# Performance work log

Measured on AMD Instinct MI355X. Metric: run time of the kernel, lower is better.

Reference implementation:

```python
import jax, jax.numpy as jnp
import numpy as np

HEADS = 4

def _topk_mask(attn, k):
    # exact replica of mask.scatter_(-1, topk_indices, 1.0): exactly k ones per row
    C = attn.shape[-1]
    _, idx = jax.lax.top_k(attn, k)                      # [b,h,C,k]
    return jax.nn.one_hot(idx, C, dtype=attn.dtype).sum(axis=-2) > 0  # [b,h,C,C] bool


def setup_inputs() -> dict:
    key = jax.random.key(0)
    ks = jax.random.split(key, 8)
    b, dim, h, w = 32, 128, 4096, 1
    s = 0.05
    return {
        "x": jax.random.normal(ks[0], (b, dim, h, w), jnp.float32),
        "qkv_w": jax.random.normal(ks[1], (3 * dim, dim), jnp.float32) * s,
        "qkv_b": jax.random.normal(ks[2], (3 * dim,), jnp.float32) * s,
        "dw_w": jax.random.normal(ks[3], (3 * dim, 1, 3, 3), jnp.float32) * s,
        "dw_b": jax.random.normal(ks[4], (3 * dim,), jnp.float32) * s,
        "proj_w": jax.random.normal(ks[5], (dim, dim), jnp.float32) * s,
        "proj_b": jax.random.normal(ks[6], (dim,), jnp.float32) * s,
        "temperature": jnp.ones((HEADS, 1, 1), jnp.float32),
        "attn_w": jnp.full((4,), 0.2, jnp.float32),  # attn1..attn4
    }


def reference(x, qkv_w, qkv_b, dw_w, dw_b, proj_w, proj_b, temperature, attn_w):
    b, c, h, w = x.shape
    # 1x1 conv qkv, then 3x3 depthwise conv (groups = 3*c)
    qkv = jnp.einsum('bchw,oc->bohw', x, qkv_w) + qkv_b[None, :, None, None]
    qkv = jax.lax.conv_general_dilated(
        qkv, dw_w, window_strides=(1, 1), padding=((1, 1), (1, 1)),
        dimension_numbers=('NCHW', 'OIHW', 'NCHW'), feature_group_count=3 * c
    ) + dw_b[None, :, None, None]
    q, k, v = jnp.split(qkv, 3, axis=1)
    heads = lambda t: t.reshape(b, HEADS, c // HEADS, h * w)  # b head c (hw)
    q, k, v = heads(q), heads(k), heads(v)
    # F.normalize(dim=-1), eps=1e-12
    q = q / jnp.maximum(jnp.linalg.norm(q, axis=-1, keepdims=True), 1e-12)
    k = k / jnp.maximum(jnp.linalg.norm(k, axis=-1, keepdims=True), 1e-12)
    C = c // HEADS
    attn = jnp.einsum('bhcn,bhdn->bhcd', q, k) * temperature[None]  # [b,head,C,C]
    top_ks = [C // 2, (2 * C) // 3, (3 * C) // 4, (4 * C) // 5]
    out = jnp.zeros_like(v)
    for i, kk in enumerate(top_ks):
        m = _topk_mask(attn, kk)
        a = jax.nn.softmax(jnp.where(m, attn, -jnp.inf), axis=-1)
        out = out + attn_w[i] * jnp.einsum('bhcd,bhdn->bhcn', a, v)
    out = out.reshape(b, c, h, w)
    out = jnp.einsum('bchw,oc->bohw', out, proj_w) + proj_b[None, :, None, None]
    return out
```

## Files before the change

### kernel.cpp

```cpp
#include <hip/hip_runtime.h>

#define B_ 32
#define CD 128
#define O3 384
#define N  4096
#define H_ 4
#define C_ 32

typedef __bf16 bf16x8 __attribute__((ext_vector_type(8)));
typedef float floatx4 __attribute__((ext_vector_type(4)));

#define MFMA16(a, b, c) __builtin_amdgcn_mfma_f32_16x16x32_bf16(a, b, c, 0, 0, 0)

__device__ __forceinline__ float b2f(unsigned int u) {
  return __builtin_bit_cast(float, u << 16);
}
__device__ __forceinline__ float b2fh(unsigned int u) {
  return __builtin_bit_cast(float, u & 0xffff0000u);
}
__device__ __forceinline__ unsigned short f2b(float f) {
  unsigned int bits = __builtin_bit_cast(unsigned int, f);
  unsigned int r = (bits + 0x7FFFu + ((bits >> 16) & 1u)) >> 16;
  return (unsigned short)r;
}

__global__ __launch_bounds__(256) void k0_xt(
    const float* __restrict__ x, unsigned short* __restrict__ xT,
    const float* __restrict__ qkv_w, const float* __restrict__ proj_w,
    const float* __restrict__ dw_w, const float* __restrict__ dw_b,
    unsigned short* __restrict__ qkv_wb, unsigned short* __restrict__ proj_wb,
    float4* __restrict__ dwq)
{
  __shared__ float xt[32 * 68];
  const int t = threadIdx.x;
  const int n0 = blockIdx.x * 64, c0 = blockIdx.y * 32, b = blockIdx.z;
  const float* xb = x + ((size_t)b * CD + c0) * N + n0;
#pragma unroll
  for (int i = 0; i < 2; i++) {
    int f = i * 256 + t;
    int c = f >> 4, n4 = (f & 15) * 4;
    float4 v = *(const float4*)(xb + (size_t)c * N + n4);
    *(float4*)&xt[c * 68 + n4] = v;
  }

  if (blockIdx.z == 0 && blockIdx.y < 2) {
    int wid = blockIdx.y * 64 + blockIdx.x;
    if (wid < 66) {
      int e = (wid * 256 + t) * 4;
      if (e < 49152) {
        float4 v = *(const float4*)(qkv_w + e);
        unsigned short tmp[4] = {f2b(v.x), f2b(v.y), f2b(v.z), f2b(v.w)};
        *(uint2*)(qkv_wb + e) = *(uint2*)tmp;
      } else if (e < 65536) {
        int off = e - 49152;
        float4 v = *(const float4*)(proj_w + off);
        unsigned short tmp[4] = {f2b(v.x), f2b(v.y), f2b(v.z), f2b(v.w)};
        *(uint2*)(proj_wb + off) = *(uint2*)tmp;
      } else {
        int o = (e - 65536) >> 2;
        if (o < 384)
          dwq[o] = make_float4(dw_w[o * 9 + 1], dw_w[o * 9 + 4],
                               dw_w[o * 9 + 7], dw_b[o]);
      }
    }
  }

  __syncthreads();
  int n = t >> 2, cb = (t & 3) * 8;
  unsigned short tmp[8];
#pragma unroll
  for (int j = 0; j < 8; j++) tmp[j] = f2b(xt[(cb + j) * 68 + n]);
  *(uint4*)(xT + ((size_t)b * N + n0 + n) * CD + c0 + cb) = *(uint4*)tmp;
}

__global__ __launch_bounds__(256, 4) void k1_qkv_dw(
    const unsigned short* __restrict__ xT, const unsigned short* __restrict__ qkv_wb,
    const float* __restrict__ qkv_b, const float4* __restrict__ dwq,
    unsigned short* __restrict__ qkvd, unsigned short* __restrict__ vT)
{
  __shared__ __align__(16) char smem[34816];
  unsigned short* Bs   = (unsigned short*)smem;
  unsigned short* pres = (unsigned short*)smem;

  const int t = threadIdx.x;
  const int otile = blockIdx.x, ytile = blockIdx.y, b = blockIdx.z;
  const int obase = otile * 128;
  const int ybase = ytile * 124;
  const int wv = t >> 6, l = t & 63, quad = l >> 4, lm = l & 15;
  const bool interior = (ytile >= 1 && ytile <= 32);

  const unsigned short* wbase =
      qkv_wb + (size_t)(obase + wv * 32 + lm) * CD + quad * 8;
  bf16x8 wa0[4], wa1[4];
#pragma unroll
  for (int ks = 0; ks < 4; ks++) {
    wa0[ks] = *(const bf16x8*)(wbase + ks * 32);
    wa1[ks] = *(const bf16x8*)(wbase + 16 * CD + ks * 32);
  }

  if (interior) {
#pragma unroll
    for (int i = 0; i < 8; i++) {
      int f = i * 256 + t;
      int row = f >> 4, c8 = (f & 15) * 8;
      *(uint4*)&Bs[row * 136 + c8] =
          *(const uint4*)(xT + ((size_t)b * N + ybase - 2 + row) * CD + c8);
    }
  } else {
#pragma unroll
    for (int i = 0; i < 8; i++) {
      int f = i * 256 + t;
      int row = f >> 4, c8 = (f & 15) * 8;
      int yg = ybase - 2 + row;
      uint4 v = make_uint4(0u, 0u, 0u, 0u);
      if (yg >= 0 && yg < N)
        v = *(const uint4*)(xT + ((size_t)b * N + yg) * CD + c8);
      *(uint4*)&Bs[row * 136 + c8] = v;
    }
  }
  __syncthreads();

  floatx4 acc[2][8];
#pragma unroll
  for (int mt = 0; mt < 2; mt++)
#pragma unroll
    for (int nt = 0; nt < 8; nt++) acc[mt][nt] = (floatx4){0.f, 0.f, 0.f, 0.f};

#pragma unroll
  for (int ks = 0; ks < 4; ks++) {
#pragma unroll
    for (int nt = 0; nt < 8; nt++) {
      bf16x8 bb = *(const bf16x8*)&Bs[(nt * 16 + lm) * 136 + ks * 32 + quad * 8];
      acc[0][nt] = MFMA16(wa0[ks], bb, acc[0][nt]);
      acc[1][nt] = MFMA16(wa1[ks], bb, acc[1][nt]);
    }
  }

  if (otile < 2) {
    __syncthreads();
    if (interior) {
#pragma unroll
      for (int mt = 0; mt < 2; mt++)
#pragma unroll
        for (int r = 0; r < 4; r++) {
          int o = wv * 32 + mt * 16 + quad * 4 + r;
          float bias = qkv_b[obase + o];
#pragma unroll
          for (int nt = 0; nt < 8; nt++) {
            int i = nt * 16 + lm;
            if (i >= 1) pres[o * 132 + (i - 1)] = f2b(acc[mt][nt][r] + bias);
          }
        }
    } else {
#pragma unroll
      for (int mt = 0; mt < 2; mt++)
#pragma unroll
        for (int r = 0; r < 4; r++) {
          int o = wv * 32 + mt * 16 + quad * 4 + r;
          float bias = qkv_b[obase + o];
#pragma unroll
          for (int nt = 0; nt < 8; nt++) {
            int i = nt * 16 + lm;
            if (i >= 1) {
              int yg = ybase - 2 + i;
              pres[o * 132 + (i - 1)] =
                  f2b((yg >= 0 && yg < N) ? (acc[mt][nt][r] + bias) : 0.f);
            }
          }
        }
    }
    __syncthreads();
    const int p = t & 63, og = t >> 6;
    const bool ok = (p < 62) && (ybase + 2 * p < N);
    const unsigned int* presu = (const unsigned int*)pres;
    for (int r2 = 0; r2 < 32; r2++) {
      int oo = __builtin_amdgcn_readfirstlane(obase + og * 32 + r2);
      float4 wq = dwq[oo];
      int o = oo - obase;
      unsigned int u0 = presu[o * 66 + p];
      unsigned int u1 = presu[o * 66 + p + 1];
      float v0 = b2f(u0), v1 = b2fh(u0), v2 = b2f(u1), v3 = b2fh(u1);
      float out0 = wq.x * v0 + wq.y * v1 + wq.z * v2 + wq.w;
      float out1 = wq.x * v1 + wq.y * v2 + wq.z * v3 + wq.w;
      unsigned int pk = (unsigned int)f2b(out0) |
                        ((unsigned int)f2b(out1) << 16);
      if (ok)
        *(unsigned int*)(qkvd + ((size_t)b * 256 + oo) * N + ybase + 2 * p) = pk;
    }
  } else {
    const int op = t & 63, quarter = t >> 6;
    const int o0 = 2 * op;
    const float4 wqa = dwq[256 + o0];
    const float4 wqb = dwq[256 + o0 + 1];
    __syncthreads();
    if (interior) {
#pragma unroll
      for (int mt = 0; mt < 2; mt++)
#pragma unroll
        for (int r = 0; r < 4; r++) {
          int o2 = wv * 32 + mt * 16 + quad * 4 + r;
          float bias = qkv_b[obase + o2];
#pragma unroll
          for (int nt = 0; nt < 8; nt++) {
            int i = nt * 16 + lm;
            pres[i * 132 + o2] = f2b(acc[mt][nt][r] + bias);
          }
        }
    } else {
#pragma unroll
      for (int mt = 0; mt < 2; mt++)
#pragma unroll
        for (int r = 0; r < 4; r++) {
          int o2 = wv * 32 + mt * 16 + quad * 4 + r;
          float bias = qkv_b[obase + o2];
#pragma unroll
          for (int nt = 0; nt < 8; nt++) {
            int i = nt * 16 + lm;
            int yg = ybase - 2 + i;
            pres[i * 132 + o2] =
                f2b((yg >= 0 && yg < N) ? (acc[mt][nt][r] + bias) : 0.f);
          }
        }
    }
    __syncthreads();
    const unsigned int* pu = (const unsigned int*)pres;
    int i0 = 2 + quarter * 31;
    unsigned int pm = pu[(i0 - 1) * 66 + op];
    unsigned int pc = pu[i0 * 66 + op];
    if (interior) {
      for (int i = i0; i < i0 + 31; i++) {
        unsigned int pp = pu[(i + 1) * 66 + op];
        int yo = ybase - 2 + i;
        float a0 = wqa.x * b2f(pm) + wqa.y * b2f(pc) + wqa.z * b2f(pp) + wqa.w;
        float a1 = wqb.x * b2fh(pm) + wqb.y * b2fh(pc) + wqb.z * b2fh(pp) + wqb.w;
        unsigned int pk = (unsigned int)f2b(a0) | ((unsigned int)f2b(a1) << 16);
        *(unsigned int*)(vT + ((size_t)b * N + yo) * CD + o0) = pk;
        pm = pc; pc = pp;
      }
    } else {
      for (int i = i0; i < i0 + 31; i++) {
        unsigned int pp = pu[(i + 1) * 66 + op];
        int yo = ybase - 2 + i;
        if (yo >= 0 && yo < N) {
          float a0 = wqa.x * b2f(pm) + wqa.y * b2f(pc) + wqa.z * b2f(pp) + wqa.w;
          float a1 = wqb.x * b2fh(pm) + wqb.y * b2fh(pc) + wqb.z * b2fh(pp) + wqb.w;
          unsigned int pk = (unsigned int)f2b(a0) | ((unsigned int)f2b(a1) << 16);
          *(unsigned int*)(vT + ((size_t)b * N + yo) * CD + o0) = pk;
        }
        pm = pc; pc = pp;
      }
    }
  }
}

__global__ __launch_bounds__(256, 4) void k3_gram(
    const unsigned short* __restrict__ qkvd, float* __restrict__ part)
{
  __shared__ float red[4 * 8 * 272];
  const int ns = blockIdx.x, h = blockIdx.y, b = blockIdx.z;
  const int t = threadIdx.x;
  const int wv = t >> 6, l = t & 63, quad = l >> 4, lm = l & 15;
  const unsigned short* qb = qkvd + ((size_t)b * 256 + h * C_) * N;
  const unsigned short* kb = qkvd + ((size_t)b * 256 + 128 + h * C_) * N;

  floatx4 acc[8];
#pragma unroll
  for (int i = 0; i < 8; i++) acc[i] = (floatx4){0.f, 0.f, 0.f, 0.f};

  const int nbase = ns * 512 + wv * 32 + quad * 8;
#pragma unroll
  for (int ch = 0; ch < 4; ch++) {
    int nc = nbase + ch * 128;
    bf16x8 a0 = *(const bf16x8*)(qb + (size_t)lm * N + nc);
    bf16x8 a1 = *(const bf16x8*)(qb + (size_t)(16 + lm) * N + nc);
    bf16x8 b0 = *(const bf16x8*)(kb + (size_t)lm * N + nc);
    bf16x8 b1 = *(const bf16x8*)(kb + (size_t)(16 + lm) * N + nc);
    acc[0] = MFMA16(a0, b0, acc[0]);
    acc[1] = MFMA16(a0, b1, acc[1]);
    acc[2] = MFMA16(a1, b0, acc[2]);
    acc[3] = MFMA16(a1, b1, acc[3]);
    acc[4] = MFMA16(a0, a0, acc[4]);
    acc[5] = MFMA16(a1, a1, acc[5]);
    acc[6] = MFMA16(b0, b0, acc[6]);
    acc[7] = MFMA16(b1, b1, acc[7]);
  }

#pragma unroll
  for (int tl = 0; tl < 8; tl++)
#pragma unroll
    for (int r = 0; r < 4; r++)
      red[wv * 2176 + tl * 272 + (quad * 4 + r) * 17 + lm] = acc[tl][r];
  __syncthreads();

  float* pb = part + ((size_t)(b * H_ + h) * 8 + ns) * 2048;
  for (int e = t; e < 2048; e += 256) {
    int tl = e >> 8, rc = e & 255, row = rc >> 4, col = rc & 15;
    int a = tl * 272 + row * 17 + col;
    float s = red[a] + red[2176 + a] + red[2 * 2176 + a] + red[3 * 2176 + a];
    if (tl < 4) {
      int mt = tl >> 1, nt = tl & 1;
      pb[(mt * 16 + row) * 32 + nt * 16 + col] = s;
    } else if (row == col) {
      if (tl < 6) pb[1024 + (tl - 4) * 16 + row] = s;
      else        pb[1056 + (tl - 6) * 16 + row] = s;
    }
  }
}

__global__ __launch_bounds__(256) void k45(
    const float* __restrict__ part, const unsigned short* __restrict__ proj_wb,
    const float* __restrict__ temperature, const float* __restrict__ attn_w,
    unsigned short* __restrict__ Mb)
{
  __shared__ float La[H_][C_][33];
  __shared__ float sq2[256];
  __shared__ float rn[256];
  __shared__ float exL[H_][C_][33];
  __shared__ unsigned char rkL[H_][C_][C_];
  __shared__ unsigned short AwtT[H_][C_][40];
  const int b = blockIdx.x, t = threadIdx.x;

  const float* pbb = part + (size_t)b * 65536;
  for (int e = t; e < 4 * 2048; e += 256) {
    int h = e >> 11, idx = e & 2047;
    if (idx < 1088) {
      const float* p = pbb + h * 16384 + idx;
      float s = 0.f;
#pragma unroll
      for (int j = 0; j < 8; j++) s += p[j * 2048];
      if (idx < 1024) La[h][idx >> 5][idx & 31] = s;
      else if (idx < 1056) sq2[h * 32 + (idx - 1024)] = s;
      else sq2[128 + h * 32 + (idx - 1056)] = s;
    }
  }
  __syncthreads();
  rn[t] = 1.f / fmaxf(sqrtf(sq2[t]), 1e-12f);
  __syncthreads();
  for (int e = t; e < 4096; e += 256) {
    int h = e >> 10, i = (e >> 5) & 31, j = e & 31;
    La[h][i][j] *= rn[h * 32 + i] * rn[128 + h * 32 + j] * temperature[h];
  }
  __syncthreads();

  if (t < 128) {
    int h = t >> 5, i = t & 31;
    float m = -1e30f;
    for (int j = 0; j < 32; j++) m = fmaxf(m, La[h][i][j]);
    float S0 = 0.f, S1 = 0.f, S2 = 0.f, S3 = 0.f;
    for (int j = 0; j < 32; j++) {
      float vj = La[h][i][j];
      int r = 0;
      for (int j2 = 0; j2 < 32; j2++) {
        float v2 = La[h][i][j2];
        r += (v2 > vj) || (v2 == vj && j2 < j);
      }
      float e = __expf(vj - m);
      exL[h][i][j] = e;
      rkL[h][i][j] = (unsigned char)r;
      if (r < 16) S0 += e;
      if (r < 21) S1 += e;
      if (r < 24) S2 += e;
      if (r < 25) S3 += e;
    }
    float w0 = attn_w[0] / S0, w1 = attn_w[1] / S1;
    float w2 = attn_w[2] / S2, w3 = attn_w[3] / S3;
    for (int j = 0; j < 32; j++) {
      int r = rkL[h][i][j];
      float cmb = (r < 16 ? w0 : 0.f) + (r < 21 ? w1 : 0.f) +
                  (r < 24 ? w2 : 0.f) + (r < 25 ? w3 : 0.f);
      AwtT[h][j][i] = f2b(exL[h][i][j] * cmb);
    }
  }
  __syncthreads();

  {
    const int wv = t >> 6, l = t & 63, quad = l >> 4, lm = l & 15;
    const int h = wv;
    bf16x8 bfr[2];
#pragma unroll
    for (int jt = 0; jt < 2; jt++)
      bfr[jt] = *(const bf16x8*)&AwtT[h][jt * 16 + lm][quad * 8];
#pragma unroll
    for (int mt = 0; mt < 8; mt++) {
      bf16x8 a = *(const bf16x8*)(proj_wb +
                    (size_t)(mt * 16 + lm) * CD + h * C_ + quad * 8);
#pragma unroll
      for (int jt = 0; jt < 2; jt++) {
        floatx4 acc = (floatx4){0.f, 0.f, 0.f, 0.f};
        acc = MFMA16(a, bfr[jt], acc);
#pragma unroll
        for (int r = 0; r < 4; r++) {
          int row = quad * 4 + r;
          Mb[(size_t)b * 16384 + (mt * 16 + row) * CD + h * C_ + jt * 16 + lm] =
              f2b(acc[r]);
        }
      }
    }
  }
}

__global__ __launch_bounds__(256, 4) void k6_out(
    const unsigned short* __restrict__ vT, const unsigned short* __restrict__ Mb,
    const float* __restrict__ proj_b, float* __restrict__ out)
{
  __shared__ unsigned short Bs[128 * 136];
  const int t = threadIdx.x;
  const int y0 = blockIdx.x * 128, b = blockIdx.y;
  const int wv = t >> 6, l = t & 63, quad = l >> 4, lm = l & 15;

#pragma unroll
  for (int i = 0; i < 8; i++) {
    int f = i * 256 + t;
    int row = f >> 4, c8 = (f & 15) * 8;
    *(uint4*)&Bs[row * 136 + c8] =
        *(const uint4*)(vT + ((size_t)b * N + y0 + row) * CD + c8);
  }
  __syncthreads();

  floatx4 acc[2][8];
#pragma unroll
  for (int mt = 0; mt < 2; mt++)
#pragma unroll
    for (int nt = 0; nt < 8; nt++) acc[mt][nt] = (floatx4){0.f, 0.f, 0.f, 0.f};

  const unsigned short* mbase =
      Mb + (size_t)b * 16384 + (size_t)(wv * 32 + lm) * CD + quad * 8;
#pragma unroll
  for (int ks = 0; ks < 4; ks++) {
    bf16x8 a0 = *(const bf16x8*)(mbase + ks * 32);
    bf16x8 a1 = *(const bf16x8*)(mbase + 16 * CD + ks * 32);
#pragma unroll
    for (int nt = 0; nt < 8; nt++) {
      bf16x8 bb = *(const bf16x8*)&Bs[(nt * 16 + lm) * 136 + ks * 32 + quad * 8];
      acc[0][nt] = MFMA16(a0, bb, acc[0][nt]);
      acc[1][nt] = MFMA16(a1, bb, acc[1][nt]);
    }
  }

#pragma unroll
  for (int mt = 0; mt < 2; mt++)
#pragma unroll
    for (int r = 0; r < 4; r++) {
      int o = wv * 32 + mt * 16 + quad * 4 + r;
      float pb = proj_b[o];
#pragma unroll
      for (int nt = 0; nt < 8; nt++) {
        int y = y0 + nt * 16 + lm;
        out[((size_t)b * CD + o) * N + y] = acc[mt][nt][r] + pb;
      }
    }
}

extern "C" void kernel_launch(void* const* d_in, const int* in_sizes, int n_in,
                              void* d_out, int out_size, void* d_ws, size_t ws_size,
                              hipStream_t stream)
{
  (void)in_sizes; (void)n_in; (void)out_size; (void)ws_size;
  const float* x           = (const float*)d_in[0];
  const float* qkv_w       = (const float*)d_in[1];
  const float* qkv_b       = (const float*)d_in[2];
  const float* dw_w        = (const float*)d_in[3];
  const float* dw_b        = (const float*)d_in[4];
  const float* proj_w      = (const float*)d_in[5];
  const float* proj_b      = (const float*)d_in[6];
  const float* temperature = (const float*)d_in[7];
  const float* attn_w      = (const float*)d_in[8];
  float* out = (float*)d_out;

  unsigned short* xT      = (unsigned short*)d_ws;
  unsigned short* qkv_wb  = xT + (size_t)16777216;
  unsigned short* proj_wb = qkv_wb + 49152;
  unsigned short* qkvd    = proj_wb + 16384;
  unsigned short* vT      = qkvd + (size_t)33554432;
  unsigned short* Mb      = vT + (size_t)16777216;
  float* part = (float*)xT;
  float4* dwq = (float4*)Mb;

  k0_xt    <<<dim3(64, 4, 32),  256, 0, stream>>>(x, xT, qkv_w, proj_w, dw_w,
                                                  dw_b, qkv_wb, proj_wb, dwq);
  k1_qkv_dw<<<dim3(3, 34, 32),  256, 0, stream>>>(xT, qkv_wb, qkv_b, dwq,
                                                  qkvd, vT);
  k3_gram  <<<dim3(8, H_, B_),  256, 0, stream>>>(qkvd, part);
  k45      <<<dim3(B_),         256, 0, stream>>>(part, proj_wb, temperature,
                                                  attn_w, Mb);
  k6_out   <<<dim3(32, B_),     256, 0, stream>>>(vT, Mb, proj_b, out);
}
```

Baseline: 251.4 us.

## Fuse Gram-matrix computation into QKV/depthwise kernel via atomics, drop qkvd round-trip

The q/k path of the QKV+depthwise kernel now computes 62-row tiles with all 256 q/k channels per block. It applies the depthwise conv in registers using lane shuffles, with the bias folded into a precomputed constant and edge corrections at the sequence ends. It then computes the per-head QK^T and squared-norm Gram partials with MFMA and atomically accumulates them into a small buffer zeroed in k0. This removes the separate k3_gram kernel, the 64MB bf16 qkvd write/read, and the 8-way partial reduction in k45. The costs are atomic contention, a lower occupancy bound, and nondeterministic float summation order.

```diff
diff --git a/kernel.cpp b/kernel.cpp
--- a/kernel.cpp
+++ b/kernel.cpp
@@ -28,8 +28,11 @@
     const float* __restrict__ x, unsigned short* __restrict__ xT,
     const float* __restrict__ qkv_w, const float* __restrict__ proj_w,
     const float* __restrict__ dw_w, const float* __restrict__ dw_b,
+    const float* __restrict__ qkv_b,
     unsigned short* __restrict__ qkv_wb, unsigned short* __restrict__ proj_wb,
-    float4* __restrict__ dwq)
+    float4* __restrict__ dwq, float4* __restrict__ dwq2,
+    float* __restrict__ c0a, float* __restrict__ c2a,
+    float* __restrict__ part2)
 {
   __shared__ float xt[32 * 68];
   const int t = threadIdx.x;
@@ -62,6 +65,18 @@
           dwq[o] = make_float4(dw_w[o * 9 + 1], dw_w[o * 9 + 4],
                                dw_w[o * 9 + 7], dw_b[o]);
       }
+    } else if (wid == 66) {
+      int o = t;
+      float w0 = dw_w[o * 9 + 1], w1 = dw_w[o * 9 + 4], w2 = dw_w[o * 9 + 7];
+      float qb = qkv_b[o];
+      dwq2[o] = make_float4(w0, w1, w2, qb * (w0 + w1 + w2) + dw_b[o]);
+      c0a[o] = qb * w0;
+      c2a[o] = qb * w2;
+    } else {
+      int idx = (wid - 67) * 256 + t;
+      uint4 z4 = make_uint4(0u, 0u, 0u, 0u);
+      for (int k2 = idx; k2 < 34816; k2 += 61 * 256)
+        ((uint4*)part2)[k2] = z4;
     }
   }
 
@@ -73,121 +88,212 @@
   *(uint4*)(xT + ((size_t)b * N + n0 + n) * CD + c0 + cb) = *(uint4*)tmp;
 }
 
-__global__ __launch_bounds__(256, 4) void k1_qkv_dw(
+__global__ __launch_bounds__(256, 3) void k1_qkv_dw(
     const unsigned short* __restrict__ xT, const unsigned short* __restrict__ qkv_wb,
     const float* __restrict__ qkv_b, const float4* __restrict__ dwq,
-    unsigned short* __restrict__ qkvd, unsigned short* __restrict__ vT)
+    const float4* __restrict__ dwq2, const float* __restrict__ c0a,
+    const float* __restrict__ c2a, unsigned short* __restrict__ vT,
+    float* part2)
 {
   __shared__ __align__(16) char smem[34816];
-  unsigned short* Bs   = (unsigned short*)smem;
-  unsigned short* pres = (unsigned short*)smem;
-
   const int t = threadIdx.x;
-  const int otile = blockIdx.x, ytile = blockIdx.y, b = blockIdx.z;
-  const int obase = otile * 128;
-  const int ybase = ytile * 124;
+  const int b = blockIdx.y;
   const int wv = t >> 6, l = t & 63, quad = l >> 4, lm = l & 15;
-  const bool interior = (ytile >= 1 && ytile <= 32);
-
-  const unsigned short* wbase =
-      qkv_wb + (size_t)(obase + wv * 32 + lm) * CD + quad * 8;
-  bf16x8 wa0[4], wa1[4];
-#pragma unroll
-  for (int ks = 0; ks < 4; ks++) {
-    wa0[ks] = *(const bf16x8*)(wbase + ks * 32);
-    wa1[ks] = *(const bf16x8*)(wbase + 16 * CD + ks * 32);
-  }
-
-  if (interior) {
-#pragma unroll
-    for (int i = 0; i < 8; i++) {
-      int f = i * 256 + t;
-      int row = f >> 4, c8 = (f & 15) * 8;
-      *(uint4*)&Bs[row * 136 + c8] =
-          *(const uint4*)(xT + ((size_t)b * N + ybase - 2 + row) * CD + c8);
+
+  if (blockIdx.x < 67) {
+    unsigned short* Bs    = (unsigned short*)smem;
+    unsigned short* pres2 = (unsigned short*)smem;
+    const int yw = blockIdx.x;
+    const int ybase = yw * 62;
+    const bool interior = (yw >= 1 && yw <= 65);
+
+    const unsigned short* wbase = qkv_wb + (size_t)(wv * 64 + lm) * CD + quad * 8;
+    bf16x8 wa[4][4];
+#pragma unroll
+    for (int mt = 0; mt < 4; mt++)
+#pragma unroll
+      for (int ks = 0; ks < 4; ks++)
+        wa[mt][ks] = *(const bf16x8*)(wbase + (size_t)mt * 16 * CD + ks * 32);
+
+    if (interior) {
+#pragma unroll
+      for (int i = 0; i < 4; i++) {
+        int f = i * 256 + t;
+        int row = f >> 4, c8 = (f & 15) * 8;
+        *(uint4*)&Bs[row * 136 + c8] =
+            *(const uint4*)(xT + ((size_t)b * N + ybase - 1 + row) * CD + c8);
+      }
+    } else {
+#pragma unroll
+      for (int i = 0; i < 4; i++) {
+        int f = i * 256 + t;
+        int row = f >> 4, c8 = (f & 15) * 8;
+        int yg = ybase - 1 + row;
+        uint4 v = make_uint4(0u, 0u, 0u, 0u);
+        if (yg >= 0 && yg < N)
+          v = *(const uint4*)(xT + ((size_t)b * N + yg) * CD + c8);
+        *(uint4*)&Bs[row * 136 + c8] = v;
+      }
+    }
+    __syncthreads();
+
+    floatx4 acc[4][4];
+#pragma unroll
+    for (int mt = 0; mt < 4; mt++)
+#pragma unroll
+      for (int nt = 0; nt < 4; nt++) acc[mt][nt] = (floatx4){0.f, 0.f, 0.f, 0.f};
+
+#pragma unroll
+    for (int ks = 0; ks < 4; ks++) {
+      bf16x8 bb[4];
+#pragma unroll
+      for (int nt = 0; nt < 4; nt++)
+        bb[nt] = *(const bf16x8*)&Bs[(nt * 16 + lm) * 136 + ks * 32 + quad * 8];
+#pragma unroll
+      for (int mt = 0; mt < 4; mt++)
+#pragma unroll
+        for (int nt = 0; nt < 4; nt++)
+          acc[mt][nt] = MFMA16(wa[mt][ks], bb[nt], acc[mt][nt]);
+    }
+    __syncthreads();
+
+    const int i1 = (l & 48) | ((lm + 1) & 15);
+    const int i2 = (l & 48) | ((lm + 2) & 15);
+#pragma unroll
+    for (int mt = 0; mt < 4; mt++) {
+#pragma unroll
+      for (int r = 0; r < 4; r++) {
+        int o = wv * 64 + mt * 16 + quad * 4 + r;
+        float4 wq = dwq2[o];
+        float cc0 = 0.f, cc2 = 0.f;
+        if (yw == 0)  cc0 = c0a[o];
+        if (yw == 66) cc2 = c2a[o];
+        float vv[5], r1[5], r2[5];
+#pragma unroll
+        for (int nt = 0; nt < 4; nt++) vv[nt] = acc[mt][nt][r];
+        vv[4] = 0.f;
+#pragma unroll
+        for (int nt = 0; nt < 4; nt++) {
+          r1[nt] = __shfl(vv[nt], i1);
+          r2[nt] = __shfl(vv[nt], i2);
+        }
+        r1[4] = 0.f; r2[4] = 0.f;
+#pragma unroll
+        for (int nt = 0; nt < 4; nt++) {
+          int p = nt * 16 + lm;
+          int y = ybase + p;
+          float g1 = (lm == 15) ? r1[nt + 1] : r1[nt];
+          float g2 = (lm >= 14) ? r2[nt + 1] : r2[nt];
+          float val = wq.x * vv[nt] + wq.y * g1 + wq.z * g2 + wq.w;
+          if (y == 0)     val -= cc0;
+          if (y == N - 1) val -= cc2;
+          bool ok = (p < 62) && (y < N);
+          pres2[o * 68 + p] = f2b(ok ? val : 0.f);
+        }
+      }
+    }
+    __syncthreads();
+
+    const int h = wv;
+    const unsigned short* pq = pres2 + (size_t)(h * 32) * 68;
+    const unsigned short* pk = pres2 + (size_t)(128 + h * 32) * 68;
+    floatx4 gqk[2][2], gqq[2], gkk[2];
+#pragma unroll
+    for (int a = 0; a < 2; a++) {
+      gqq[a] = (floatx4){0.f, 0.f, 0.f, 0.f};
+      gkk[a] = (floatx4){0.f, 0.f, 0.f, 0.f};
+#pragma unroll
+      for (int c = 0; c < 2; c++) gqk[a][c] = (floatx4){0.f, 0.f, 0.f, 0.f};
+    }
+#pragma unroll
+    for (int kc = 0; kc < 2; kc++) {
+      bf16x8 qf[2], kf[2];
+#pragma unroll
+      for (int tt = 0; tt < 2; tt++) {
+        qf[tt] = *(const bf16x8*)&pq[(tt * 16 + lm) * 68 + kc * 32 + quad * 8];
+        kf[tt] = *(const bf16x8*)&pk[(tt * 16 + lm) * 68 + kc * 32 + quad * 8];
+      }
+#pragma unroll
+      for (int tq = 0; tq < 2; tq++)
+#pragma unroll
+        for (int tk = 0; tk < 2; tk++)
+          gqk[tq][tk] = MFMA16(qf[tq], kf[tk], gqk[tq][tk]);
+      gqq[0] = MFMA16(qf[0], qf[0], gqq[0]);
+      gqq[1] = MFMA16(qf[1], qf[1], gqq[1]);
+      gkk[0] = MFMA16(kf[0], kf[0], gkk[0]);
+      gkk[1] = MFMA16(kf[1], kf[1], gkk[1]);
+    }
+    float* pp = part2 + ((size_t)b * H_ + h) * 1088;
+#pragma unroll
+    for (int tq = 0; tq < 2; tq++)
+#pragma unroll
+      for (int tk = 0; tk < 2; tk++)
+#pragma unroll
+        for (int r = 0; r < 4; r++)
+          atomicAdd(&pp[(tq * 16 + quad * 4 + r) * 32 + tk * 16 + lm],
+                    gqk[tq][tk][r]);
+    if (quad == (lm >> 2)) {
+      int r = lm & 3;
+      atomicAdd(&pp[1024 + lm],      gqq[0][r]);
+      atomicAdd(&pp[1024 + 16 + lm], gqq[1][r]);
+      atomicAdd(&pp[1056 + lm],      gkk[0][r]);
+      atomicAdd(&pp[1056 + 16 + lm], gkk[1][r]);
     }
   } else {
-#pragma unroll
-    for (int i = 0; i < 8; i++) {
-      int f = i * 256 + t;
-      int row = f >> 4, c8 = (f & 15) * 8;
-      int yg = ybase - 2 + row;
-      uint4 v = make_uint4(0u, 0u, 0u, 0u);
-      if (yg >= 0 && yg < N)
-        v = *(const uint4*)(xT + ((size_t)b * N + yg) * CD + c8);
-      *(uint4*)&Bs[row * 136 + c8] = v;
-    }
-  }
-  __syncthreads();
-
-  floatx4 acc[2][8];
-#pragma unroll
-  for (int mt = 0; mt < 2; mt++)
-#pragma unroll
-    for (int nt = 0; nt < 8; nt++) acc[mt][nt] = (floatx4){0.f, 0.f, 0.f, 0.f};
-
-#pragma unroll
-  for (int ks = 0; ks < 4; ks++) {
-#pragma unroll
-    for (int nt = 0; nt < 8; nt++) {
-      bf16x8 bb = *(const bf16x8*)&Bs[(nt * 16 + lm) * 136 + ks * 32 + quad * 8];
-      acc[0][nt] = MFMA16(wa0[ks], bb, acc[0][nt]);
-      acc[1][nt] = MFMA16(wa1[ks], bb, acc[1][nt]);
-    }
-  }
-
-  if (otile < 2) {
+    unsigned short* Bs   = (unsigned short*)smem;
+    unsigned short* pres = (unsigned short*)smem;
+    const int ytile = blockIdx.x - 67;
+    const int obase = 256;
+    const int ybase = ytile * 124;
+    const bool interior = (ytile >= 1 && ytile <= 32);
+
+    const unsigned short* wbase =
+        qkv_wb + (size_t)(obase + wv * 32 + lm) * CD + quad * 8;
+    bf16x8 wa0[4], wa1[4];
+#pragma unroll
+    for (int ks = 0; ks < 4; ks++) {
+      wa0[ks] = *(const bf16x8*)(wbase + ks * 32);
+      wa1[ks] = *(const bf16x8*)(wbase + 16 * CD + ks * 32);
+    }
+
+    if (interior) {
+#pragma unroll
+      for (int i = 0; i < 8; i++) {
+        int f = i * 256 + t;
+        int row = f >> 4, c8 = (f & 15) * 8;
+        *(uint4*)&Bs[row * 136 + c8] =
+            *(const uint4*)(xT + ((size_t)b * N + ybase - 2 + row) * CD + c8);
+      }
+    } else {
+#pragma unroll
+      for (int i = 0; i < 8; i++) {
+        int f = i * 256 + t;
+        int row = f >> 4, c8 = (f & 15) * 8;
+        int yg = ybase - 2 + row;
+        uint4 v = make_uint4(0u, 0u, 0u, 0u);
+        if (yg >= 0 && yg < N)
+          v = *(const uint4*)(xT + ((size_t)b * N + yg) * CD + c8);
+        *(uint4*)&Bs[row * 136 + c8] = v;
+      }
+    }
     __syncthreads();
-    if (interior) {
-#pragma unroll
-      for (int mt = 0; mt < 2; mt++)
-#pragma unroll
-        for (int r = 0; r < 4; r++) {
-          int o = wv * 32 + mt * 16 + quad * 4 + r;
-          float bias = qkv_b[obase + o];
-#pragma unroll
-          for (int nt = 0; nt < 8; nt++) {
-            int i = nt * 16 + lm;
-            if (i >= 1) pres[o * 132 + (i - 1)] = f2b(acc[mt][nt][r] + bias);
-          }
-        }
-    } else {
-#pragma unroll
-      for (int mt = 0; mt < 2; mt++)
-#pragma unroll
-        for (int r = 0; r < 4; r++) {
-          int o = wv * 32 + mt * 16 + quad * 4 + r;
-          float bias = qkv_b[obase + o];
-#pragma unroll
-          for (int nt = 0; nt < 8; nt++) {
-            int i = nt * 16 + lm;
-            if (i >= 1) {
-              int yg = ybase - 2 + i;
-              pres[o * 132 + (i - 1)] =
-                  f2b((yg >= 0 && yg < N) ? (acc[mt][nt][r] + bias) : 0.f);
-            }
-          }
-        }
-    }
-    __syncthreads();
-    const int p = t & 63, og = t >> 6;
-    const bool ok = (p < 62) && (ybase + 2 * p < N);
-    const unsigned int* presu = (const unsigned int*)pres;
-    for (int r2 = 0; r2 < 32; r2++) {
-      int oo = __builtin_amdgcn_readfirstlane(obase + og * 32 + r2);
-      float4 wq = dwq[oo];
-      int o = oo - obase;
-      unsigned int u0 = presu[o * 66 + p];
-      unsigned int u1 = presu[o * 66 + p + 1];
-      float v0 = b2f(u0), v1 = b2fh(u0), v2 = b2f(u1), v3 = b2fh(u1);
-      float out0 = wq.x * v0 + wq.y * v1 + wq.z * v2 + wq.w;
-      float out1 = wq.x * v1 + wq.y * v2 + wq.z * v3 + wq.w;
-      unsigned int pk = (unsigned int)f2b(out0) |
-                        ((unsigned int)f2b(out1) << 16);
-      if (ok)
-        *(unsigned int*)(qkvd + ((size_t)b * 256 + oo) * N + ybase + 2 * p) = pk;
-    }
-  } else {
+
+    floatx4 acc[2][8];
+#pragma unroll
+    for (int mt = 0; mt < 2; mt++)
+#pragma unroll
+      for (int nt = 0; nt < 8; nt++) acc[mt][nt] = (floatx4){0.f, 0.f, 0.f, 0.f};
+
+#pragma unroll
+    for (int ks = 0; ks < 4; ks++) {
+#pragma unroll
+      for (int nt = 0; nt < 8; nt++) {
+        bf16x8 bb = *(const bf16x8*)&Bs[(nt * 16 + lm) * 136 + ks * 32 + quad * 8];
+        acc[0][nt] = MFMA16(wa0[ks], bb, acc[0][nt]);
+        acc[1][nt] = MFMA16(wa1[ks], bb, acc[1][nt]);
+      }
+    }
+
     const int op = t & 63, quarter = t >> 6;
     const int o0 = 2 * op;
     const float4 wqa = dwq[256 + o0];
@@ -229,86 +335,32 @@
     unsigned int pc = pu[i0 * 66 + op];
     if (interior) {
       for (int i = i0; i < i0 + 31; i++) {
-        unsigned int pp = pu[(i + 1) * 66 + op];
+        unsigned int pp2 = pu[(i + 1) * 66 + op];
         int yo = ybase - 2 + i;
-        float a0 = wqa.x * b2f(pm) + wqa.y * b2f(pc) + wqa.z * b2f(pp) + wqa.w;
-        float a1 = wqb.x * b2fh(pm) + wqb.y * b2fh(pc) + wqb.z * b2fh(pp) + wqb.w;
-        unsigned int pk = (unsigned int)f2b(a0) | ((unsigned int)f2b(a1) << 16);
-        *(unsigned int*)(vT + ((size_t)b * N + yo) * CD + o0) = pk;
-        pm = pc; pc = pp;
+        float a0 = wqa.x * b2f(pm) + wqa.y * b2f(pc) + wqa.z * b2f(pp2) + wqa.w;
+        float a1 = wqb.x * b2fh(pm) + wqb.y * b2fh(pc) + wqb.z * b2fh(pp2) + wqb.w;
+        unsigned int pk2 = (unsigned int)f2b(a0) | ((unsigned int)f2b(a1) << 16);
+        *(unsigned int*)(vT + ((size_t)b * N + yo) * CD + o0) = pk2;
+        pm = pc; pc = pp2;
       }
     } else {
       for (int i = i0; i < i0 + 31; i++) {
-        unsigned int pp = pu[(i + 1) * 66 + op];
+        unsigned int pp2 = pu[(i + 1) * 66 + op];
         int yo = ybase - 2 + i;
         if (yo >= 0 && yo < N) {
-          float a0 = wqa.x * b2f(pm) + wqa.y * b2f(pc) + wqa.z * b2f(pp) + wqa.w;
-          float a1 = wqb.x * b2fh(pm) + wqb.y * b2fh(pc) + wqb.z * b2fh(pp) + wqb.w;
-          unsigned int pk = (unsigned int)f2b(a0) | ((unsigned int)f2b(a1) << 16);
-          *(unsigned int*)(vT + ((size_t)b * N + yo) * CD + o0) = pk;
+          float a0 = wqa.x * b2f(pm) + wqa.y * b2f(pc) + wqa.z * b2f(pp2) + wqa.w;
+          float a1 = wqb.x * b2fh(pm) + wqb.y * b2fh(pc) + wqb.z * b2fh(pp2) + wqb.w;
+          unsigned int pk2 = (unsigned int)f2b(a0) | ((unsigned int)f2b(a1) << 16);
+          *(unsigned int*)(vT + ((size_t)b * N + yo) * CD + o0) = pk2;
         }
-        pm = pc; pc = pp;
-      }
-    }
-  }
-}
-
-__global__ __launch_bounds__(256, 4) void k3_gram(
-    const unsigned short* __restrict__ qkvd, float* __restrict__ part)
-{
-  __shared__ float red[4 * 8 * 272];
-  const int ns = blockIdx.x, h = blockIdx.y, b = blockIdx.z;
-  const int t = threadIdx.x;
-  const int wv = t >> 6, l = t & 63, quad = l >> 4, lm = l & 15;
-  const unsigned short* qb = qkvd + ((size_t)b * 256 + h * C_) * N;
-  const unsigned short* kb = qkvd + ((size_t)b * 256 + 128 + h * C_) * N;
-
-  floatx4 acc[8];
-#pragma unroll
-  for (int i = 0; i < 8; i++) acc[i] = (floatx4){0.f, 0.f, 0.f, 0.f};
-
-  const int nbase = ns * 512 + wv * 32 + quad * 8;
-#pragma unroll
-  for (int ch = 0; ch < 4; ch++) {
-    int nc = nbase + ch * 128;
-    bf16x8 a0 = *(const bf16x8*)(qb + (size_t)lm * N + nc);
-    bf16x8 a1 = *(const bf16x8*)(qb + (size_t)(16 + lm) * N + nc);
-    bf16x8 b0 = *(const bf16x8*)(kb + (size_t)lm * N + nc);
-    bf16x8 b1 = *(const bf16x8*)(kb + (size_t)(16 + lm) * N + nc);
-    acc[0] = MFMA16(a0, b0, acc[0]);
-    acc[1] = MFMA16(a0, b1, acc[1]);
-    acc[2] = MFMA16(a1, b0, acc[2]);
-    acc[3] = MFMA16(a1, b1, acc[3]);
-    acc[4] = MFMA16(a0, a0, acc[4]);
-    acc[5] = MFMA16(a1, a1, acc[5]);
-    acc[6] = MFMA16(b0, b0, acc[6]);
-    acc[7] = MFMA16(b1, b1, acc[7]);
-  }
-
-#pragma unroll
-  for (int tl = 0; tl < 8; tl++)
-#pragma unroll
-    for (int r = 0; r < 4; r++)
-      red[wv * 2176 + tl * 272 + (quad * 4 + r) * 17 + lm] = acc[tl][r];
-  __syncthreads();
-
-  float* pb = part + ((size_t)(b * H_ + h) * 8 + ns) * 2048;
-  for (int e = t; e < 2048; e += 256) {
-    int tl = e >> 8, rc = e & 255, row = rc >> 4, col = rc & 15;
-    int a = tl * 272 + row * 17 + col;
-    float s = red[a] + red[2176 + a] + red[2 * 2176 + a] + red[3 * 2176 + a];
-    if (tl < 4) {
-      int mt = tl >> 1, nt = tl & 1;
-      pb[(mt * 16 + row) * 32 + nt * 16 + col] = s;
-    } else if (row == col) {
-      if (tl < 6) pb[1024 + (tl - 4) * 16 + row] = s;
-      else        pb[1056 + (tl - 6) * 16 + row] = s;
+        pm = pc; pc = pp2;
+      }
     }
   }
 }
 
 __global__ __launch_bounds__(256) void k45(
-    const float* __restrict__ part, const unsigned short* __restrict__ proj_wb,
+    const float* __restrict__ part2, const unsigned short* __restrict__ proj_wb,
     const float* __restrict__ temperature, const float* __restrict__ attn_w,
     unsigned short* __restrict__ Mb)
 {
@@ -320,19 +372,15 @@
   __shared__ unsigned short AwtT[H_][C_][40];
   const int b = blockIdx.x, t = threadIdx.x;
 
-  const float* pbb = part + (size_t)b * 65536;
-  for (int e = t; e < 4 * 2048; e += 256) {
-    int h = e >> 11, idx = e & 2047;
-    if (idx < 1088) {
-      const float* p = pbb + h * 16384 + idx;
-      float s = 0.f;
-#pragma unroll
-      for (int j = 0; j < 8; j++) s += p[j * 2048];
+  const float* pbb = part2 + (size_t)b * H_ * 1088;
+#pragma unroll
+  for (int h = 0; h < H_; h++)
+    for (int idx = t; idx < 1088; idx += 256) {
+      float s = pbb[h * 1088 + idx];
       if (idx < 1024) La[h][idx >> 5][idx & 31] = s;
       else if (idx < 1056) sq2[h * 32 + (idx - 1024)] = s;
       else sq2[128 + h * 32 + (idx - 1056)] = s;
     }
-  }
   __syncthreads();
   rn[t] = 1.f / fmaxf(sqrtf(sq2[t]), 1e-12f);
   __syncthreads();
@@ -470,18 +518,21 @@
   unsigned short* xT      = (unsigned short*)d_ws;
   unsigned short* qkv_wb  = xT + (size_t)16777216;
   unsigned short* proj_wb = qkv_wb + 49152;
-  unsigned short* qkvd    = proj_wb + 16384;
-  unsigned short* vT      = qkvd + (size_t)33554432;
+  unsigned short* hole    = proj_wb + 16384;
+  unsigned short* vT      = hole + (size_t)33554432;
   unsigned short* Mb      = vT + (size_t)16777216;
-  float* part = (float*)xT;
-  float4* dwq = (float4*)Mb;
-
-  k0_xt    <<<dim3(64, 4, 32),  256, 0, stream>>>(x, xT, qkv_w, proj_w, dw_w,
-                                                  dw_b, qkv_wb, proj_wb, dwq);
-  k1_qkv_dw<<<dim3(3, 34, 32),  256, 0, stream>>>(xT, qkv_wb, qkv_b, dwq,
-                                                  qkvd, vT);
-  k3_gram  <<<dim3(8, H_, B_),  256, 0, stream>>>(qkvd, part);
-  k45      <<<dim3(B_),         256, 0, stream>>>(part, proj_wb, temperature,
-                                                  attn_w, Mb);
-  k6_out   <<<dim3(32, B_),     256, 0, stream>>>(vT, Mb, proj_b, out);
-}
+  float* part2 = (float*)(Mb + 524288);
+  float4* dwq  = (float4*)Mb;
+  float4* dwq2 = (float4*)(Mb + 3072);
+  float*  c0a  = (float*)(Mb + 5120);
+  float*  c2a  = (float*)(Mb + 5632);
+
+  k0_xt    <<<dim3(64, 4, 32), 256, 0, stream>>>(x, xT, qkv_w, proj_w, dw_w,
+                                                 dw_b, qkv_b, qkv_wb, proj_wb,
+                                                 dwq, dwq2, c0a, c2a, part2);
+  k1_qkv_dw<<<dim3(101, 32),   256, 0, stream>>>(xT, qkv_wb, qkv_b, dwq, dwq2,
+                                                 c0a, c2a, vT, part2);
+  k45      <<<dim3(B_),        256, 0, stream>>>(part2, proj_wb, temperature,
+                                                 attn_w, Mb);
+  k6_out   <<<dim3(32, B_),    256, 0, stream>>>(vT, Mb, proj_b, out);
+}
```

Result: faster. 234.9 us (-6.6%).
